# Kernel optimization log

Hardware: AMD Instinct MI355X
Metric: run time of the kernel (lower is better)

## Reference

```python
import jax, jax.numpy as jnp
import numpy as np
import math

B, S, IN_DIM, EMBED, H = 4, 2048, 1024, 1024, 16
HD = EMBED // H

def setup_inputs() -> dict:
    key = jax.random.key(0)
    ks = jax.random.split(key, 8)
    scale = 0.02
    return {
        "q": jax.random.normal(ks[0], (B, S, IN_DIM), jnp.float32),
        "k": jax.random.normal(ks[1], (B, S, IN_DIM), jnp.float32),
        "v": jax.random.normal(ks[2], (B, S, IN_DIM), jnp.float32),
        "mask": jnp.ones((B, 1, S, S), jnp.int32),
        "Wk": jax.random.normal(ks[3], (EMBED, IN_DIM), jnp.float32) * scale,
        "bk": jnp.zeros((EMBED,), jnp.float32),
        "Wv": jax.random.normal(ks[4], (EMBED, IN_DIM), jnp.float32) * scale,
        "bv": jnp.zeros((EMBED,), jnp.float32),
        "Wo": jax.random.normal(ks[5], (IN_DIM, EMBED), jnp.float32) * scale,
        "bo": jnp.zeros((IN_DIM,), jnp.float32),
    }

def _split_heads(x):
    # [B,S,E] -> [B,H,S,HD]
    b, s, _ = x.shape
    return x.reshape(b, s, H, HD).transpose(0, 2, 1, 3)

def reference(q, k, v, mask, Wk, bk, Wv, bv, Wo, bo):
    # NOTE: faithful to the original bug: q is projected with Wv, not Wq.
    vp = _split_heads(v @ Wv.T + bv)
    kp = _split_heads(k @ Wk.T + bk)
    qp = _split_heads(q @ Wv.T + bv)
    score = jnp.einsum('bhqd,bhkd->bhqk', qp, kp) / math.sqrt(HD)
    score = jnp.where(mask == 0, -jnp.inf, score)
    attn = jax.nn.softmax(score, axis=-1)
    ctx = jnp.einsum('bhqk,bhkd->bhqd', attn, vp)
    ctx = ctx.transpose(0, 2, 1, 3).reshape(q.shape[0], q.shape[1], EMBED)
    out = ctx @ Wo.T + bo
    return (out, attn)
```

## Files before the change

### kernel.cpp

```cpp
#include <hip/hip_runtime.h>
#include <stdint.h>

typedef unsigned short u16;
typedef unsigned int u32;
typedef float f32x4 __attribute__((ext_vector_type(4)));
typedef __bf16 bf16x8 __attribute__((ext_vector_type(8)));
typedef u16 u16x8 __attribute__((ext_vector_type(8)));
typedef u16 u16x4 __attribute__((ext_vector_type(4)));

#define NB   4
#define SEQ  2048
#define EMB  1024
#define NH   16
#define HDIM 64

#define QSCALE 0.18033688011112042f

__device__ __forceinline__ f32x4 mfma16(bf16x8 a, bf16x8 b, f32x4 c) {
  return __builtin_amdgcn_mfma_f32_16x16x32_bf16(a, b, c, 0, 0, 0);
}
__device__ __forceinline__ u16 f2bf(float f) {
  u32 u = __builtin_bit_cast(u32, f);
  u += 0x7FFFu + ((u >> 16) & 1u);
  return (u16)(u >> 16);
}
__device__ __forceinline__ u32 pk2bf(float lo, float hi) {
  return (u32)f2bf(lo) | ((u32)f2bf(hi) << 16);
}
__device__ __forceinline__ float bf2f(u16 h) {
  return __builtin_bit_cast(float, (u32)h << 16);
}
__device__ __forceinline__ bf16x8 ldg8(const u16* p) {
  return *reinterpret_cast<const bf16x8*>(p);
}

__global__ __launch_bounds__(256) void prep_kernel(
    const float* __restrict__ q, const float* __restrict__ k, const float* __restrict__ v,
    const float* __restrict__ Wk, const float* __restrict__ Wv, const float* __restrict__ Wo,
    const int* __restrict__ mask,
    u16* __restrict__ qb, u16* __restrict__ kb, u16* __restrict__ vb,
    u16* __restrict__ Wkb, u16* __restrict__ Wvb, u16* __restrict__ Wob,
    u32* __restrict__ bits) {
  const int y = blockIdx.y;
  if (y == 6) {
    const int idx = blockIdx.x * 256 + threadIdx.x;
    if (idx >= NB * SEQ * 64) return;
    const int w = idx & 63;
    const size_t rowbase = (size_t)(idx >> 6) * SEQ;
    const int4* p = reinterpret_cast<const int4*>(mask + rowbase + w * 32);
    u32 m = 0;
#pragma unroll
    for (int j = 0; j < 8; ++j) {
      int4 v4 = p[j];
      m |= (v4.x != 0 ? 1u : 0u) << (j * 4 + 0);
      m |= (v4.y != 0 ? 1u : 0u) << (j * 4 + 1);
      m |= (v4.z != 0 ? 1u : 0u) << (j * 4 + 2);
      m |= (v4.w != 0 ? 1u : 0u) << (j * 4 + 3);
    }
    bits[idx] = m;
    return;
  }
  const float* src; u16* dst; int n8;
  switch (y) {
    case 0: src = q;  dst = qb;  n8 = NB * SEQ * EMB / 8; break;
    case 1: src = k;  dst = kb;  n8 = NB * SEQ * EMB / 8; break;
    case 2: src = v;  dst = vb;  n8 = NB * SEQ * EMB / 8; break;
    case 3: src = Wk; dst = Wkb; n8 = EMB * EMB / 8; break;
    case 4: src = Wv; dst = Wvb; n8 = EMB * EMB / 8; break;
    default: src = Wo; dst = Wob; n8 = EMB * EMB / 8; break;
  }
  int i = blockIdx.x * 256 + threadIdx.x;
  if (i >= n8) return;
  const float4* s = reinterpret_cast<const float4*>(src) + (size_t)i * 2;
  float4 a = s[0], b = s[1];
  u16x8 o;
  o[0] = f2bf(a.x); o[1] = f2bf(a.y); o[2] = f2bf(a.z); o[3] = f2bf(a.w);
  o[4] = f2bf(b.x); o[5] = f2bf(b.y); o[6] = f2bf(b.z); o[7] = f2bf(b.w);
  reinterpret_cast<u16x8*>(dst)[i] = o;
}

__global__ __launch_bounds__(256) void tileok_kernel(const u32* __restrict__ bits,
                                                     unsigned char* __restrict__ tok) {
  const int idx = blockIdx.x * 256 + threadIdx.x;
  const int b = idx >> 10, qt = (idx >> 5) & 31, kt = idx & 31;
  const u32* bb = bits + (size_t)b * SEQ * 64;
  u32 acc = 0xFFFFFFFFu;
  for (int rr = 0; rr < 64; ++rr) {
    const u32* pr = bb + (size_t)(qt * 64 + rr) * 64 + kt * 2;
    acc &= pr[0] & pr[1];
  }
  tok[idx] = (acc == 0xFFFFFFFFu) ? 1 : 0;
}

__device__ __forceinline__ void gemm_tile(const u16* __restrict__ A,
                                          const u16* __restrict__ W,
                                          int brow, int bcol, int tid,
                                          u16* As, u16* Bs, f32x4 acc[4][4]) {
  const int K = 1024;
  const int l = tid & 63, wv = tid >> 6;
  const int lr = l & 15, lg = l >> 4;
  const int wr = wv >> 1, wc = wv & 1;
  const int srow = l >> 3;
  const int skb = (l & 7) * 16;

  for (int k0 = 0; k0 < K; k0 += 64) {
#pragma unroll
    for (int r = 0; r < 4; ++r) {
      const int chunk = r * 4 + wv;
      const int row = chunk * 8 + srow;
      const char* ga = (const char*)A + ((size_t)(brow + row) * K + k0) * 2 + skb;
      const char* gb = (const char*)W + ((size_t)(bcol + row) * K + k0) * 2 + skb;
      __builtin_amdgcn_global_load_lds(
          (const __attribute__((address_space(1))) u32*)ga,
          (__attribute__((address_space(3))) u32*)((char*)As + chunk * 1024), 16, 0, 0);
      __builtin_amdgcn_global_load_lds(
          (const __attribute__((address_space(1))) u32*)gb,
          (__attribute__((address_space(3))) u32*)((char*)Bs + chunk * 1024), 16, 0, 0);
    }
    __syncthreads();
#pragma unroll
    for (int ks = 0; ks < 2; ++ks) {
      bf16x8 af[4], bfr[4];
#pragma unroll
      for (int m = 0; m < 4; ++m)
        af[m] = *reinterpret_cast<const bf16x8*>(
            (const char*)As + (wr * 64 + m * 16 + lr) * 128 + ks * 64 + lg * 16);
#pragma unroll
      for (int n = 0; n < 4; ++n)
        bfr[n] = *reinterpret_cast<const bf16x8*>(
            (const char*)Bs + (wc * 64 + n * 16 + lr) * 128 + ks * 64 + lg * 16);
#pragma unroll
      for (int m = 0; m < 4; ++m)
#pragma unroll
        for (int n = 0; n < 4; ++n)
          acc[m][n] = mfma16(af[m], bfr[n], acc[m][n]);
    }
    __syncthreads();
  }
}

__global__ __launch_bounds__(256) void proj_gemm(
    const u16* __restrict__ qb, const u16* __restrict__ kb, const u16* __restrict__ vb,
    const u16* __restrict__ Wvb, const u16* __restrict__ Wkb,
    const float* __restrict__ bv, const float* __restrict__ bkp,
    u16* __restrict__ qp, u16* __restrict__ kp, u16* __restrict__ vpT) {
  __shared__ __align__(16) u32 smem_u32[8192];
  u16* As = (u16*)smem_u32;
  u16* Bs = As + 128 * 64;
  const int z = blockIdx.z;
  const u16* A = (z == 0) ? qb : (z == 1) ? kb : vb;
  const u16* W = (z == 1) ? Wkb : Wvb;
  const float* bias = (z == 1) ? bkp : bv;
  const int brow = blockIdx.y * 128;
  const int bcol = blockIdx.x * 128;
  const int tid = threadIdx.x;
  f32x4 acc[4][4] = {};
  gemm_tile(A, W, brow, bcol, tid, As, Bs, acc);
  const int l = tid & 63, wv = tid >> 6;
  const int lr = l & 15, lg = l >> 4;
  const int wr = wv >> 1, wc = wv & 1;

  if (z == 2) {
#pragma unroll
    for (int m = 0; m < 4; ++m)
#pragma unroll
      for (int n = 0; n < 4; ++n) {
        const int cl = wc * 64 + n * 16 + lr;
        const float b0 = bias[bcol + cl];
        const u32 w0 = pk2bf(acc[m][n][0] + b0, acc[m][n][1] + b0);
        const u32 w1 = pk2bf(acc[m][n][2] + b0, acc[m][n][3] + b0);
        const int rp0 = wr * 32 + m * 8 + lg * 2;
        const int a32 = cl * 64 + (rp0 ^ ((lr & 7) << 2));
        uint2 wv2; wv2.x = w0; wv2.y = w1;
        *reinterpret_cast<uint2*>(&smem_u32[a32]) = wv2;
      }
    __syncthreads();
#pragma unroll
    for (int i = 0; i < 8; ++i) {
      const int idx = i * 256 + tid;
      const int cl = idx >> 4;
      const int rp0 = (idx & 15) * 4;
      const int a32 = cl * 64 + (rp0 ^ ((cl & 7) << 2));
      const uint4 d = *reinterpret_cast<const uint4*>(&smem_u32[a32]);
      const int col = bcol + cl, hh = col >> 6, hd = col & 63;
      const int row = brow + rp0 * 2, bb = row >> 11, s = row & 2047;
      *reinterpret_cast<uint4*>(
          vpT + ((((size_t)bb * NH + hh) * HDIM + hd) * SEQ + s)) = d;
    }
  } else {
    u16* dst = (z == 0) ? qp : kp;
    const float sc = (z == 0) ? QSCALE : 1.0f;
#pragma unroll
    for (int m = 0; m < 4; ++m)
#pragma unroll
      for (int n = 0; n < 4; ++n)
#pragma unroll
        for (int r = 0; r < 4; ++r) {
          const int row = brow + wr * 64 + m * 16 + lg * 4 + r;
          const int col = bcol + wc * 64 + n * 16 + lr;
          const float vl = (acc[m][n][r] + bias[col]) * sc;
          const int bb = row >> 11, s = row & 2047, hh = col >> 6, hd = col & 63;
          dst[(((size_t)bb * NH + hh) * SEQ + s) * HDIM + hd] = f2bf(vl);
        }
  }
}

__global__ __launch_bounds__(256) void out_gemm(
    const u16* __restrict__ ctxb, const u16* __restrict__ Wob,
    const float* __restrict__ bo, float* __restrict__ outF) {
  __shared__ __align__(16) u32 smem_u32[8192];
  u16* As = (u16*)smem_u32;
  u16* Bs = As + 128 * 64;
  const int brow = blockIdx.y * 128;
  const int bcol = blockIdx.x * 128;
  const int tid = threadIdx.x;
  f32x4 acc[4][4] = {};
  gemm_tile(ctxb, Wob, brow, bcol, tid, As, Bs, acc);
  const int l = tid & 63, wv = tid >> 6;
  const int lr = l & 15, lg = l >> 4;
  const int wr = wv >> 1, wc = wv & 1;
#pragma unroll
  for (int m = 0; m < 4; ++m)
#pragma unroll
    for (int n = 0; n < 4; ++n)
#pragma unroll
      for (int r = 0; r < 4; ++r) {
        const int row = brow + wr * 64 + m * 16 + lg * 4 + r;
        const int col = bcol + wc * 64 + n * 16 + lr;
        outF[(size_t)row * EMB + col] = acc[m][n][r] + bo[col];
      }
}

__global__ __launch_bounds__(256) void attn_kernel(
    const u16* __restrict__ qp, const u16* __restrict__ kp, const u16* __restrict__ vpT,
    const u32* __restrict__ bits, const unsigned char* __restrict__ tok,
    float* __restrict__ attn, u16* __restrict__ ctxb) {
  __shared__ __align__(16) u16 pbuf[4][32][64];
  const int tid = threadIdx.x;
  const int l = tid & 63, wid = tid >> 6;
  const int lr = l & 15, lg = l >> 4;
  const int bid = blockIdx.x;
  const int swz = (bid & 7) * 128 + (bid >> 3);
  const int Wn = swz * 4 + wid;
  const int qt = Wn & 63, h = (Wn >> 6) & 15, b = Wn >> 10;
  const int q0 = qt * 32;
  const size_t bh = (size_t)b * NH + h;
  const u16* qpb = qp + bh * (SEQ * HDIM);
  const u16* kpb = kp + bh * (SEQ * HDIM);
  const u16* vpb = vpT + bh * (HDIM * SEQ);
  float* attb = attn + bh * ((size_t)SEQ * SEQ);
  const unsigned char* tokb = tok + ((size_t)b * 32 + (qt >> 1)) * 32;
  const u32* bitsb = bits + (size_t)b * SEQ * 64;

  bf16x8 aq[2][2];
#pragma unroll
  for (int g = 0; g < 2; ++g)
#pragma unroll
    for (int d = 0; d < 2; ++d)
      aq[g][d] = ldg8(qpb + (size_t)(q0 + g * 16 + lr) * HDIM + d * 32 + lg * 8);

  float sums[2][4] = {{0.f, 0.f, 0.f, 0.f}, {0.f, 0.f, 0.f, 0.f}};
  for (int kt = 0; kt < 32; ++kt) {
    const int kc = kt * 64;
    const bool okt = tokb[kt] != 0;
    bf16x8 bk8[4][2];
#pragma unroll
    for (int st = 0; st < 4; ++st)
#pragma unroll
      for (int d = 0; d < 2; ++d)
        bk8[st][d] = ldg8(kpb + (size_t)(kc + st * 16 + lr) * HDIM + d * 32 + lg * 8);
#pragma unroll
    for (int g = 0; g < 2; ++g)
#pragma unroll
      for (int st = 0; st < 4; ++st) {
        f32x4 s = {0.f, 0.f, 0.f, 0.f};
        s = mfma16(aq[g][0], bk8[st][0], s);
        s = mfma16(aq[g][1], bk8[st][1], s);
#pragma unroll
        for (int r = 0; r < 4; ++r) {
          float sc = s[r];
          if (!okt) {
            const int qrow = q0 + g * 16 + lg * 4 + r;
            const int kpos = kc + st * 16 + lr;
            const u32 wb = bitsb[(size_t)qrow * 64 + (kpos >> 5)];
            if (!((wb >> (kpos & 31)) & 1u)) sc = -1e30f;
          }
          sums[g][r] += __builtin_amdgcn_exp2f(sc);
        }
      }
  }
  float rinv[2][4];
#pragma unroll
  for (int g = 0; g < 2; ++g)
#pragma unroll
    for (int r = 0; r < 4; ++r) {
      float vsum = sums[g][r];
      vsum += __shfl_xor(vsum, 1);
      vsum += __shfl_xor(vsum, 2);
      vsum += __shfl_xor(vsum, 4);
      vsum += __shfl_xor(vsum, 8);
      rinv[g][r] = 1.0f / vsum;
    }

  f32x4 cacc[2][4] = {};
  for (int kt = 0; kt < 32; ++kt) {
    const int kc = kt * 64;
    const bool okt = tokb[kt] != 0;
    bf16x8 bk8[4][2];
#pragma unroll
    for (int st = 0; st < 4; ++st)
#pragma unroll
      for (int d = 0; d < 2; ++d)
        bk8[st][d] = ldg8(kpb + (size_t)(kc + st * 16 + lr) * HDIM + d * 32 + lg * 8);
#pragma unroll
    for (int g = 0; g < 2; ++g)
#pragma unroll
      for (int st = 0; st < 4; ++st) {
        f32x4 s = {0.f, 0.f, 0.f, 0.f};
        s = mfma16(aq[g][0], bk8[st][0], s);
        s = mfma16(aq[g][1], bk8[st][1], s);
#pragma unroll
        for (int r = 0; r < 4; ++r) {
          float sc = s[r];
          if (!okt) {
            const int qrow = q0 + g * 16 + lg * 4 + r;
            const int kpos = kc + st * 16 + lr;
            const u32 wb = bitsb[(size_t)qrow * 64 + (kpos >> 5)];
            if (!((wb >> (kpos & 31)) & 1u)) sc = -1e30f;
          }
          const float pn = __builtin_amdgcn_exp2f(sc) * rinv[g][r];
          const int row = g * 16 + lg * 4 + r;
          const int col = st * 16 + lr;
          pbuf[wid][row][col ^ ((row & 7) << 3)] = f2bf(pn);
        }
      }
    bf16x8 vf[4][2];
#pragma unroll
    for (int ds = 0; ds < 4; ++ds)
#pragma unroll
      for (int x = 0; x < 2; ++x)
        vf[ds][x] = ldg8(vpb + (size_t)(ds * 16 + lr) * SEQ + kc + x * 32 + lg * 8);
#pragma unroll
    for (int g = 0; g < 2; ++g)
#pragma unroll
      for (int ks = 0; ks < 2; ++ks) {
        const int prow = g * 16 + lr;
        const int cb = ks * 32 + lg * 8;
        const bf16x8 pa = *reinterpret_cast<const bf16x8*>(
            &pbuf[wid][prow][cb ^ ((prow & 7) << 3)]);
#pragma unroll
        for (int ds = 0; ds < 4; ++ds)
          cacc[g][ds] = mfma16(pa, vf[ds][ks], cacc[g][ds]);
      }
#pragma unroll
    for (int i = 0; i < 8; ++i) {
      const int row = i * 4 + lg;
      const int c4 = (l & 15) * 4;
      const u16x4 raw = *reinterpret_cast<const u16x4*>(
          &pbuf[wid][row][c4 ^ ((row & 7) << 3)]);
      f32x4 o;
      o[0] = bf2f(raw[0]); o[1] = bf2f(raw[1]);
      o[2] = bf2f(raw[2]); o[3] = bf2f(raw[3]);
      __builtin_nontemporal_store(
          o, reinterpret_cast<f32x4*>(attb + (size_t)(q0 + row) * SEQ + kc + c4));
    }
  }

#pragma unroll
  for (int g = 0; g < 2; ++g)
#pragma unroll
    for (int ds = 0; ds < 4; ++ds)
#pragma unroll
      for (int r = 0; r < 4; ++r)
        ctxb[((size_t)b * SEQ + q0 + g * 16 + lg * 4 + r) * EMB + h * HDIM + ds * 16 + lr] =
            f2bf(cacc[g][ds][r]);
}

extern "C" void kernel_launch(void* const* d_in, const int* in_sizes, int n_in,
                              void* d_out, int out_size, void* d_ws, size_t ws_size,
                              hipStream_t stream) {
  const float* q   = (const float*)d_in[0];
  const float* k   = (const float*)d_in[1];
  const float* v   = (const float*)d_in[2];
  const int* mask  = (const int*)d_in[3];
  const float* Wk  = (const float*)d_in[4];
  const float* bk  = (const float*)d_in[5];
  const float* Wv  = (const float*)d_in[6];
  const float* bv  = (const float*)d_in[7];
  const float* Wo  = (const float*)d_in[8];
  const float* bo  = (const float*)d_in[9];

  float* outF = (float*)d_out;
  float* attnF = outF + (size_t)NB * SEQ * EMB;

  const size_t MiB = 1024 * 1024;
  char* ws = (char*)d_ws;
  u16* qb   = (u16*)(ws + 0 * MiB);
  u16* kb   = (u16*)(ws + 16 * MiB);
  u16* vb   = (u16*)(ws + 32 * MiB);
  u16* Wvb  = (u16*)(ws + 48 * MiB);
  u16* Wkb  = (u16*)(ws + 50 * MiB);
  u16* Wob  = (u16*)(ws + 52 * MiB);
  u16* qpB  = (u16*)(ws + 54 * MiB);
  u16* kpB  = (u16*)(ws + 70 * MiB);
  u16* vpT  = (u16*)(ws + 86 * MiB);
  u16* ctxb = (u16*)(ws + 102 * MiB);
  u32* bits = (u32*)(ws + 118 * MiB);
  unsigned char* tok = (unsigned char*)(ws + 120 * MiB);

  prep_kernel<<<dim3(NB * SEQ * EMB / 8 / 256, 7), 256, 0, stream>>>(
      q, k, v, Wk, Wv, Wo, mask, qb, kb, vb, Wkb, Wvb, Wob, bits);

  tileok_kernel<<<NB * 32 * 32 / 256, 256, 0, stream>>>(bits, tok);

  proj_gemm<<<dim3(EMB / 128, NB * SEQ / 128, 3), 256, 0, stream>>>(
      qb, kb, vb, Wvb, Wkb, bv, bk, qpB, kpB, vpT);

  attn_kernel<<<1024, 256, 0, stream>>>(
      qpB, kpB, vpT, bits, tok, attnF, ctxb);

  out_gemm<<<dim3(EMB / 128, NB * SEQ / 128), 256, 0, stream>>>(ctxb, Wob, bo, outF);
}
```

Measured before the change: 531.7 us.

## Split attention key range across four waves with shared-memory row-sum and context reduction

Each block now handles one 32-row query tile for one (batch, head). Its four waves each take a quarter of the key range instead of each wave owning a separate query tile, and the grid grows fourfold. Softmax row sums and partial context accumulators are combined across waves through shared memory, with block barriers in between. This raises parallelism and gives each wave a shorter serial loop, so latency is hidden better. It costs extra syncs and LDS traffic, and K loads are no longer shared across query tiles within a block.

```diff
diff --git a/kernel.cpp b/kernel.cpp
--- a/kernel.cpp
+++ b/kernel.cpp
@@ -236,14 +236,16 @@
     const u32* __restrict__ bits, const unsigned char* __restrict__ tok,
     float* __restrict__ attn, u16* __restrict__ ctxb) {
   __shared__ __align__(16) u16 pbuf[4][32][64];
+  __shared__ float rs[4][32];
+  float* red = (float*)pbuf;
   const int tid = threadIdx.x;
   const int l = tid & 63, wid = tid >> 6;
   const int lr = l & 15, lg = l >> 4;
   const int bid = blockIdx.x;
-  const int swz = (bid & 7) * 128 + (bid >> 3);
-  const int Wn = swz * 4 + wid;
-  const int qt = Wn & 63, h = (Wn >> 6) & 15, b = Wn >> 10;
+  const int bh_i = bid & 63;
+  const int qt = bid >> 6;
   const int q0 = qt * 32;
+  const int h = bh_i & 15, b = bh_i >> 4;
   const size_t bh = (size_t)b * NH + h;
   const u16* qpb = qp + bh * (SEQ * HDIM);
   const u16* kpb = kp + bh * (SEQ * HDIM);
@@ -251,6 +253,7 @@
   float* attb = attn + bh * ((size_t)SEQ * SEQ);
   const unsigned char* tokb = tok + ((size_t)b * 32 + (qt >> 1)) * 32;
   const u32* bitsb = bits + (size_t)b * SEQ * 64;
+  const int kbase = wid * 512;
 
   bf16x8 aq[2][2];
 #pragma unroll
@@ -260,9 +263,9 @@
       aq[g][d] = ldg8(qpb + (size_t)(q0 + g * 16 + lr) * HDIM + d * 32 + lg * 8);
 
   float sums[2][4] = {{0.f, 0.f, 0.f, 0.f}, {0.f, 0.f, 0.f, 0.f}};
-  for (int kt = 0; kt < 32; ++kt) {
-    const int kc = kt * 64;
-    const bool okt = tokb[kt] != 0;
+  for (int sub = 0; sub < 8; ++sub) {
+    const int kc = kbase + sub * 64;
+    const bool okt = tokb[kc >> 6] != 0;
     bf16x8 bk8[4][2];
 #pragma unroll
     for (int st = 0; st < 4; ++st)
@@ -289,7 +292,6 @@
         }
       }
   }
-  float rinv[2][4];
 #pragma unroll
   for (int g = 0; g < 2; ++g)
 #pragma unroll
@@ -299,13 +301,22 @@
       vsum += __shfl_xor(vsum, 2);
       vsum += __shfl_xor(vsum, 4);
       vsum += __shfl_xor(vsum, 8);
-      rinv[g][r] = 1.0f / vsum;
+      if (lr == 0) rs[wid][g * 16 + lg * 4 + r] = vsum;
+    }
+  __syncthreads();
+  float rinv[2][4];
+#pragma unroll
+  for (int g = 0; g < 2; ++g)
+#pragma unroll
+    for (int r = 0; r < 4; ++r) {
+      const int row = g * 16 + lg * 4 + r;
+      rinv[g][r] = 1.0f / (rs[0][row] + rs[1][row] + rs[2][row] + rs[3][row]);
     }
 
   f32x4 cacc[2][4] = {};
-  for (int kt = 0; kt < 32; ++kt) {
-    const int kc = kt * 64;
-    const bool okt = tokb[kt] != 0;
+  for (int sub = 0; sub < 8; ++sub) {
+    const int kc = kbase + sub * 64;
+    const bool okt = tokb[kc >> 6] != 0;
     bf16x8 bk8[4][2];
 #pragma unroll
     for (int st = 0; st < 4; ++st)
@@ -367,13 +378,27 @@
   }
 
 #pragma unroll
-  for (int g = 0; g < 2; ++g)
+  for (int g = 0; g < 2; ++g) {
 #pragma unroll
     for (int ds = 0; ds < 4; ++ds)
 #pragma unroll
       for (int r = 0; r < 4; ++r)
-        ctxb[((size_t)b * SEQ + q0 + g * 16 + lg * 4 + r) * EMB + h * HDIM + ds * 16 + lr] =
-            f2bf(cacc[g][ds][r]);
+        red[(wid * 16 + lg * 4 + r) * 64 + ds * 16 + lr] = cacc[g][ds][r];
+    __syncthreads();
+    {
+      const int col = tid & 63, rq = tid >> 6;
+#pragma unroll
+      for (int rr = 0; rr < 4; ++rr) {
+        const int row16 = rq + rr * 4;
+        const float tot = red[(0 * 16 + row16) * 64 + col] +
+                          red[(1 * 16 + row16) * 64 + col] +
+                          red[(2 * 16 + row16) * 64 + col] +
+                          red[(3 * 16 + row16) * 64 + col];
+        ctxb[((size_t)b * SEQ + q0 + g * 16 + row16) * EMB + h * HDIM + col] = f2bf(tot);
+      }
+    }
+    __syncthreads();
+  }
 }
 
 extern "C" void kernel_launch(void* const* d_in, const int* in_sizes, int n_in,
@@ -416,7 +441,7 @@
   proj_gemm<<<dim3(EMB / 128, NB * SEQ / 128, 3), 256, 0, stream>>>(
       qb, kb, vb, Wvb, Wkb, bv, bk, qpB, kpB, vpT);
 
-  attn_kernel<<<1024, 256, 0, stream>>>(
+  attn_kernel<<<4096, 256, 0, stream>>>(
       qpB, kpB, vpT, bits, tok, attnF, ctxb);
 
   out_gemm<<<dim3(EMB / 128, NB * SEQ / 128), 256, 0, stream>>>(ctxb, Wob, bo, outF);
```

Measured after the change: 555.8 us. 1.05x slower.

## Share K/V tiles across waves via LDS with direct global-to-LDS loads

Applied to the files above, without the earlier changes.

Each block now covers 128 consecutive query rows of one (batch, head), with its four waves sharing a single K tile (and a V tile in the second pass). Tiles are staged through swizzled LDS using global_load_lds and barriers, instead of every wave fetching K/V from global memory on its own. The block index mapping changes so that all four waves work on the same head. The attention-matrix store also drops the nontemporal hint and becomes a plain store. Per-tile barriers are added with no double buffering, so load latency is no longer hidden behind compute, and the write pattern for the large attn output changes.

```diff
diff --git a/kernel.cpp b/kernel.cpp
--- a/kernel.cpp
+++ b/kernel.cpp
@@ -235,21 +235,23 @@
     const u16* __restrict__ qp, const u16* __restrict__ kp, const u16* __restrict__ vpT,
     const u32* __restrict__ bits, const unsigned char* __restrict__ tok,
     float* __restrict__ attn, u16* __restrict__ ctxb) {
+  __shared__ __align__(16) u16 Ks[4096];
+  __shared__ __align__(16) u16 Vs[4096];
   __shared__ __align__(16) u16 pbuf[4][32][64];
   const int tid = threadIdx.x;
   const int l = tid & 63, wid = tid >> 6;
   const int lr = l & 15, lg = l >> 4;
   const int bid = blockIdx.x;
-  const int swz = (bid & 7) * 128 + (bid >> 3);
-  const int Wn = swz * 4 + wid;
-  const int qt = Wn & 63, h = (Wn >> 6) & 15, b = Wn >> 10;
-  const int q0 = qt * 32;
+  const int bh_i = bid & 63;
+  const int qg = bid >> 6;
+  const int h = bh_i & 15, b = bh_i >> 4;
+  const int q0w = qg * 128 + wid * 32;
   const size_t bh = (size_t)b * NH + h;
   const u16* qpb = qp + bh * (SEQ * HDIM);
   const u16* kpb = kp + bh * (SEQ * HDIM);
   const u16* vpb = vpT + bh * (HDIM * SEQ);
   float* attb = attn + bh * ((size_t)SEQ * SEQ);
-  const unsigned char* tokb = tok + ((size_t)b * 32 + (qt >> 1)) * 32;
+  const unsigned char* tokb = tok + ((size_t)b * 32 + (q0w >> 6)) * 32;
   const u32* bitsb = bits + (size_t)b * SEQ * 64;
 
   bf16x8 aq[2][2];
@@ -257,18 +259,33 @@
   for (int g = 0; g < 2; ++g)
 #pragma unroll
     for (int d = 0; d < 2; ++d)
-      aq[g][d] = ldg8(qpb + (size_t)(q0 + g * 16 + lr) * HDIM + d * 32 + lg * 8);
+      aq[g][d] = ldg8(qpb + (size_t)(q0w + g * 16 + lr) * HDIM + d * 32 + lg * 8);
 
   float sums[2][4] = {{0.f, 0.f, 0.f, 0.f}, {0.f, 0.f, 0.f, 0.f}};
   for (int kt = 0; kt < 32; ++kt) {
     const int kc = kt * 64;
+#pragma unroll
+    for (int c = 0; c < 2; ++c) {
+      const int gi = c * 256 + tid;
+      const int row = gi >> 3, cs = gi & 7;
+      const int csx = cs ^ (row & 7);
+      __builtin_amdgcn_global_load_lds(
+          (const __attribute__((address_space(1))) u32*)
+              ((const char*)(kpb + (size_t)(kc + row) * HDIM) + csx * 16),
+          (__attribute__((address_space(3))) u32*)((char*)Ks + c * 4096 + wid * 1024),
+          16, 0, 0);
+    }
+    __syncthreads();
     const bool okt = tokb[kt] != 0;
     bf16x8 bk8[4][2];
 #pragma unroll
     for (int st = 0; st < 4; ++st)
 #pragma unroll
-      for (int d = 0; d < 2; ++d)
-        bk8[st][d] = ldg8(kpb + (size_t)(kc + st * 16 + lr) * HDIM + d * 32 + lg * 8);
+      for (int d = 0; d < 2; ++d) {
+        const int row = st * 16 + lr;
+        bk8[st][d] = *reinterpret_cast<const bf16x8*>(
+            Ks + (((row << 3) | ((d * 4 + lg) ^ (row & 7))) << 3));
+      }
 #pragma unroll
     for (int g = 0; g < 2; ++g)
 #pragma unroll
@@ -280,7 +297,7 @@
         for (int r = 0; r < 4; ++r) {
           float sc = s[r];
           if (!okt) {
-            const int qrow = q0 + g * 16 + lg * 4 + r;
+            const int qrow = q0w + g * 16 + lg * 4 + r;
             const int kpos = kc + st * 16 + lr;
             const u32 wb = bitsb[(size_t)qrow * 64 + (kpos >> 5)];
             if (!((wb >> (kpos & 31)) & 1u)) sc = -1e30f;
@@ -288,6 +305,7 @@
           sums[g][r] += __builtin_amdgcn_exp2f(sc);
         }
       }
+    __syncthreads();
   }
   float rinv[2][4];
 #pragma unroll
@@ -305,13 +323,33 @@
   f32x4 cacc[2][4] = {};
   for (int kt = 0; kt < 32; ++kt) {
     const int kc = kt * 64;
+#pragma unroll
+    for (int c = 0; c < 2; ++c) {
+      const int gi = c * 256 + tid;
+      const int row = gi >> 3, cs = gi & 7;
+      const int csx = cs ^ (row & 7);
+      __builtin_amdgcn_global_load_lds(
+          (const __attribute__((address_space(1))) u32*)
+              ((const char*)(kpb + (size_t)(kc + row) * HDIM) + csx * 16),
+          (__attribute__((address_space(3))) u32*)((char*)Ks + c * 4096 + wid * 1024),
+          16, 0, 0);
+      __builtin_amdgcn_global_load_lds(
+          (const __attribute__((address_space(1))) u32*)
+              ((const char*)(vpb + (size_t)row * SEQ + kc) + csx * 16),
+          (__attribute__((address_space(3))) u32*)((char*)Vs + c * 4096 + wid * 1024),
+          16, 0, 0);
+    }
+    __syncthreads();
     const bool okt = tokb[kt] != 0;
     bf16x8 bk8[4][2];
 #pragma unroll
     for (int st = 0; st < 4; ++st)
 #pragma unroll
-      for (int d = 0; d < 2; ++d)
-        bk8[st][d] = ldg8(kpb + (size_t)(kc + st * 16 + lr) * HDIM + d * 32 + lg * 8);
+      for (int d = 0; d < 2; ++d) {
+        const int row = st * 16 + lr;
+        bk8[st][d] = *reinterpret_cast<const bf16x8*>(
+            Ks + (((row << 3) | ((d * 4 + lg) ^ (row & 7))) << 3));
+      }
 #pragma unroll
     for (int g = 0; g < 2; ++g)
 #pragma unroll
@@ -323,7 +361,7 @@
         for (int r = 0; r < 4; ++r) {
           float sc = s[r];
           if (!okt) {
-            const int qrow = q0 + g * 16 + lg * 4 + r;
+            const int qrow = q0w + g * 16 + lg * 4 + r;
             const int kpos = kc + st * 16 + lr;
             const u32 wb = bitsb[(size_t)qrow * 64 + (kpos >> 5)];
             if (!((wb >> (kpos & 31)) & 1u)) sc = -1e30f;
@@ -338,8 +376,11 @@
 #pragma unroll
     for (int ds = 0; ds < 4; ++ds)
 #pragma unroll
-      for (int x = 0; x < 2; ++x)
-        vf[ds][x] = ldg8(vpb + (size_t)(ds * 16 + lr) * SEQ + kc + x * 32 + lg * 8);
+      for (int x = 0; x < 2; ++x) {
+        const int row = ds * 16 + lr;
+        vf[ds][x] = *reinterpret_cast<const bf16x8*>(
+            Vs + (((row << 3) | ((x * 4 + lg) ^ (row & 7))) << 3));
+      }
 #pragma unroll
     for (int g = 0; g < 2; ++g)
 #pragma unroll
@@ -361,9 +402,9 @@
       f32x4 o;
       o[0] = bf2f(raw[0]); o[1] = bf2f(raw[1]);
       o[2] = bf2f(raw[2]); o[3] = bf2f(raw[3]);
-      __builtin_nontemporal_store(
-          o, reinterpret_cast<f32x4*>(attb + (size_t)(q0 + row) * SEQ + kc + c4));
-    }
+      *reinterpret_cast<f32x4*>(attb + (size_t)(q0w + row) * SEQ + kc + c4) = o;
+    }
+    __syncthreads();
   }
 
 #pragma unroll
@@ -372,7 +413,7 @@
     for (int ds = 0; ds < 4; ++ds)
 #pragma unroll
       for (int r = 0; r < 4; ++r)
-        ctxb[((size_t)b * SEQ + q0 + g * 16 + lg * 4 + r) * EMB + h * HDIM + ds * 16 + lr] =
+        ctxb[((size_t)b * SEQ + q0w + g * 16 + lg * 4 + r) * EMB + h * HDIM + ds * 16 + lr] =
             f2bf(cacc[g][ds][r]);
 }
 
```

Measured after the change: 628.6 us. 18.2% more time.

## Double per-wave query tile and software-pipeline K tile loads in attention

Applied to the files above, without the earlier changes.

Each wave now handles 64 query rows instead of 32, so every K/V tile fetched from global memory is reused across twice as many MFMAs, and the grid shrinks to 512 blocks. K tiles are double-buffered in registers so the next tile's loads are issued before the current tile's compute. Block mapping changes so the 4 waves of a block share the same batch-head, which improves cache locality for K/V. The cost is higher register and LDS pressure (larger accumulators, two K buffers, doubled pbuf) and fewer waves in flight, which may reduce occupancy.

```diff
diff --git a/kernel.cpp b/kernel.cpp
--- a/kernel.cpp
+++ b/kernel.cpp
@@ -235,63 +235,75 @@
     const u16* __restrict__ qp, const u16* __restrict__ kp, const u16* __restrict__ vpT,
     const u32* __restrict__ bits, const unsigned char* __restrict__ tok,
     float* __restrict__ attn, u16* __restrict__ ctxb) {
-  __shared__ __align__(16) u16 pbuf[4][32][64];
+  __shared__ __align__(16) u16 pbuf[4][64][64];
   const int tid = threadIdx.x;
   const int l = tid & 63, wid = tid >> 6;
   const int lr = l & 15, lg = l >> 4;
   const int bid = blockIdx.x;
-  const int swz = (bid & 7) * 128 + (bid >> 3);
-  const int Wn = swz * 4 + wid;
-  const int qt = Wn & 63, h = (Wn >> 6) & 15, b = Wn >> 10;
-  const int q0 = qt * 32;
+  const int bh_i = bid & 63;
+  const int qt = (bid >> 6) * 4 + wid;
+  const int q0 = qt * 64;
+  const int h = bh_i & 15, b = bh_i >> 4;
   const size_t bh = (size_t)b * NH + h;
   const u16* qpb = qp + bh * (SEQ * HDIM);
   const u16* kpb = kp + bh * (SEQ * HDIM);
   const u16* vpb = vpT + bh * (HDIM * SEQ);
   float* attb = attn + bh * ((size_t)SEQ * SEQ);
-  const unsigned char* tokb = tok + ((size_t)b * 32 + (qt >> 1)) * 32;
+  const unsigned char* tokb = tok + ((size_t)b * 32 + (q0 >> 6)) * 32;
   const u32* bitsb = bits + (size_t)b * SEQ * 64;
 
-  bf16x8 aq[2][2];
-#pragma unroll
-  for (int g = 0; g < 2; ++g)
+  bf16x8 aq[4][2];
+#pragma unroll
+  for (int g = 0; g < 4; ++g)
 #pragma unroll
     for (int d = 0; d < 2; ++d)
       aq[g][d] = ldg8(qpb + (size_t)(q0 + g * 16 + lr) * HDIM + d * 32 + lg * 8);
 
-  float sums[2][4] = {{0.f, 0.f, 0.f, 0.f}, {0.f, 0.f, 0.f, 0.f}};
-  for (int kt = 0; kt < 32; ++kt) {
-    const int kc = kt * 64;
-    const bool okt = tokb[kt] != 0;
-    bf16x8 bk8[4][2];
+  auto load_ktile = [&](int kc, bf16x8 (&kf)[4][2]) {
 #pragma unroll
     for (int st = 0; st < 4; ++st)
 #pragma unroll
       for (int d = 0; d < 2; ++d)
-        bk8[st][d] = ldg8(kpb + (size_t)(kc + st * 16 + lr) * HDIM + d * 32 + lg * 8);
-#pragma unroll
-    for (int g = 0; g < 2; ++g)
-#pragma unroll
-      for (int st = 0; st < 4; ++st) {
-        f32x4 s = {0.f, 0.f, 0.f, 0.f};
-        s = mfma16(aq[g][0], bk8[st][0], s);
-        s = mfma16(aq[g][1], bk8[st][1], s);
-#pragma unroll
-        for (int r = 0; r < 4; ++r) {
-          float sc = s[r];
-          if (!okt) {
-            const int qrow = q0 + g * 16 + lg * 4 + r;
-            const int kpos = kc + st * 16 + lr;
-            const u32 wb = bitsb[(size_t)qrow * 64 + (kpos >> 5)];
-            if (!((wb >> (kpos & 31)) & 1u)) sc = -1e30f;
+        kf[st][d] = ldg8(kpb + (size_t)(kc + st * 16 + lr) * HDIM + d * 32 + lg * 8);
+  };
+
+  float sums[4][4] = {};
+  {
+    bf16x8 kfA[4][2], kfB[4][2];
+    load_ktile(0, kfA);
+    auto p1_body = [&](int kt, const bf16x8 (&kf)[4][2]) {
+      const int kc = kt * 64;
+      const bool okt = tokb[kt] != 0;
+#pragma unroll
+      for (int g = 0; g < 4; ++g)
+#pragma unroll
+        for (int st = 0; st < 4; ++st) {
+          f32x4 s = {0.f, 0.f, 0.f, 0.f};
+          s = mfma16(aq[g][0], kf[st][0], s);
+          s = mfma16(aq[g][1], kf[st][1], s);
+#pragma unroll
+          for (int r = 0; r < 4; ++r) {
+            float sc = s[r];
+            if (!okt) {
+              const int qrow = q0 + g * 16 + lg * 4 + r;
+              const int kpos = kc + st * 16 + lr;
+              const u32 wb = bitsb[(size_t)qrow * 64 + (kpos >> 5)];
+              if (!((wb >> (kpos & 31)) & 1u)) sc = -1e30f;
+            }
+            sums[g][r] += __builtin_amdgcn_exp2f(sc);
           }
-          sums[g][r] += __builtin_amdgcn_exp2f(sc);
         }
-      }
-  }
-  float rinv[2][4];
-#pragma unroll
-  for (int g = 0; g < 2; ++g)
+    };
+    for (int kt2 = 0; kt2 < 32; kt2 += 2) {
+      load_ktile((kt2 + 1) * 64, kfB);
+      p1_body(kt2, kfA);
+      if (kt2 + 2 < 32) load_ktile((kt2 + 2) * 64, kfA);
+      p1_body(kt2 + 1, kfB);
+    }
+  }
+  float rinv[4][4];
+#pragma unroll
+  for (int g = 0; g < 4; ++g)
 #pragma unroll
     for (int r = 0; r < 4; ++r) {
       float vsum = sums[g][r];
@@ -302,72 +314,76 @@
       rinv[g][r] = 1.0f / vsum;
     }
 
-  f32x4 cacc[2][4] = {};
-  for (int kt = 0; kt < 32; ++kt) {
-    const int kc = kt * 64;
-    const bool okt = tokb[kt] != 0;
-    bf16x8 bk8[4][2];
-#pragma unroll
-    for (int st = 0; st < 4; ++st)
-#pragma unroll
-      for (int d = 0; d < 2; ++d)
-        bk8[st][d] = ldg8(kpb + (size_t)(kc + st * 16 + lr) * HDIM + d * 32 + lg * 8);
-#pragma unroll
-    for (int g = 0; g < 2; ++g)
-#pragma unroll
-      for (int st = 0; st < 4; ++st) {
-        f32x4 s = {0.f, 0.f, 0.f, 0.f};
-        s = mfma16(aq[g][0], bk8[st][0], s);
-        s = mfma16(aq[g][1], bk8[st][1], s);
-#pragma unroll
-        for (int r = 0; r < 4; ++r) {
-          float sc = s[r];
-          if (!okt) {
-            const int qrow = q0 + g * 16 + lg * 4 + r;
-            const int kpos = kc + st * 16 + lr;
-            const u32 wb = bitsb[(size_t)qrow * 64 + (kpos >> 5)];
-            if (!((wb >> (kpos & 31)) & 1u)) sc = -1e30f;
+  f32x4 cacc[4][4] = {};
+  {
+    bf16x8 kfA[4][2], kfB[4][2];
+    load_ktile(0, kfA);
+    auto p2_body = [&](int kt, const bf16x8 (&kf)[4][2]) {
+      const int kc = kt * 64;
+      const bool okt = tokb[kt] != 0;
+      bf16x8 vf[4][2];
+#pragma unroll
+      for (int ds = 0; ds < 4; ++ds)
+#pragma unroll
+        for (int x = 0; x < 2; ++x)
+          vf[ds][x] = ldg8(vpb + (size_t)(ds * 16 + lr) * SEQ + kc + x * 32 + lg * 8);
+#pragma unroll
+      for (int g = 0; g < 4; ++g)
+#pragma unroll
+        for (int st = 0; st < 4; ++st) {
+          f32x4 s = {0.f, 0.f, 0.f, 0.f};
+          s = mfma16(aq[g][0], kf[st][0], s);
+          s = mfma16(aq[g][1], kf[st][1], s);
+#pragma unroll
+          for (int r = 0; r < 4; ++r) {
+            float sc = s[r];
+            if (!okt) {
+              const int qrow = q0 + g * 16 + lg * 4 + r;
+              const int kpos = kc + st * 16 + lr;
+              const u32 wb = bitsb[(size_t)qrow * 64 + (kpos >> 5)];
+              if (!((wb >> (kpos & 31)) & 1u)) sc = -1e30f;
+            }
+            const float pn = __builtin_amdgcn_exp2f(sc) * rinv[g][r];
+            const int row = g * 16 + lg * 4 + r;
+            const int col = st * 16 + lr;
+            pbuf[wid][row][col ^ ((row & 7) << 3)] = f2bf(pn);
           }
-          const float pn = __builtin_amdgcn_exp2f(sc) * rinv[g][r];
-          const int row = g * 16 + lg * 4 + r;
-          const int col = st * 16 + lr;
-          pbuf[wid][row][col ^ ((row & 7) << 3)] = f2bf(pn);
         }
+#pragma unroll
+      for (int g = 0; g < 4; ++g)
+#pragma unroll
+        for (int ks = 0; ks < 2; ++ks) {
+          const int prow = g * 16 + lr;
+          const int cb = ks * 32 + lg * 8;
+          const bf16x8 pa = *reinterpret_cast<const bf16x8*>(
+              &pbuf[wid][prow][cb ^ ((prow & 7) << 3)]);
+#pragma unroll
+          for (int ds = 0; ds < 4; ++ds)
+            cacc[g][ds] = mfma16(pa, vf[ds][ks], cacc[g][ds]);
+        }
+#pragma unroll
+      for (int i = 0; i < 16; ++i) {
+        const int row = i * 4 + lg;
+        const int c4 = (l & 15) * 4;
+        const u16x4 raw = *reinterpret_cast<const u16x4*>(
+            &pbuf[wid][row][c4 ^ ((row & 7) << 3)]);
+        f32x4 o;
+        o[0] = bf2f(raw[0]); o[1] = bf2f(raw[1]);
+        o[2] = bf2f(raw[2]); o[3] = bf2f(raw[3]);
+        __builtin_nontemporal_store(
+            o, reinterpret_cast<f32x4*>(attb + (size_t)(q0 + row) * SEQ + kc + c4));
       }
-    bf16x8 vf[4][2];
-#pragma unroll
-    for (int ds = 0; ds < 4; ++ds)
-#pragma unroll
-      for (int x = 0; x < 2; ++x)
-        vf[ds][x] = ldg8(vpb + (size_t)(ds * 16 + lr) * SEQ + kc + x * 32 + lg * 8);
-#pragma unroll
-    for (int g = 0; g < 2; ++g)
-#pragma unroll
-      for (int ks = 0; ks < 2; ++ks) {
-        const int prow = g * 16 + lr;
-        const int cb = ks * 32 + lg * 8;
-        const bf16x8 pa = *reinterpret_cast<const bf16x8*>(
-            &pbuf[wid][prow][cb ^ ((prow & 7) << 3)]);
-#pragma unroll
-        for (int ds = 0; ds < 4; ++ds)
-          cacc[g][ds] = mfma16(pa, vf[ds][ks], cacc[g][ds]);
-      }
-#pragma unroll
-    for (int i = 0; i < 8; ++i) {
-      const int row = i * 4 + lg;
-      const int c4 = (l & 15) * 4;
-      const u16x4 raw = *reinterpret_cast<const u16x4*>(
-          &pbuf[wid][row][c4 ^ ((row & 7) << 3)]);
-      f32x4 o;
-      o[0] = bf2f(raw[0]); o[1] = bf2f(raw[1]);
-      o[2] = bf2f(raw[2]); o[3] = bf2f(raw[3]);
-      __builtin_nontemporal_store(
-          o, reinterpret_cast<f32x4*>(attb + (size_t)(q0 + row) * SEQ + kc + c4));
-    }
-  }
-
-#pragma unroll
-  for (int g = 0; g < 2; ++g)
+    };
+    for (int kt2 = 0; kt2 < 32; kt2 += 2) {
+      load_ktile((kt2 + 1) * 64, kfB);
+      p2_body(kt2, kfA);
+      if (kt2 + 2 < 32) load_ktile((kt2 + 2) * 64, kfA);
+      p2_body(kt2 + 1, kfB);
+    }
+  }
+
+#pragma unroll
+  for (int g = 0; g < 4; ++g)
 #pragma unroll
     for (int ds = 0; ds < 4; ++ds)
 #pragma unroll
@@ -416,7 +432,7 @@
   proj_gemm<<<dim3(EMB / 128, NB * SEQ / 128, 3), 256, 0, stream>>>(
       qb, kb, vb, Wvb, Wkb, bv, bk, qpB, kpB, vpT);
 
-  attn_kernel<<<1024, 256, 0, stream>>>(
+  attn_kernel<<<512, 256, 0, stream>>>(
       qpB, kpB, vpT, bits, tok, attnF, ctxb);
 
   out_gemm<<<dim3(EMB / 128, NB * SEQ / 128), 256, 0, stream>>>(ctxb, Wob, bo, outF);
```

Result: slower. 591.7 us (+11.3%).
